# Optimization experiments

Hardware: AMD Instinct MI355X
Metric: run time of the kernel (lower is better)

## Reference

```python
import jax, jax.numpy as jnp
import numpy as np

N, S, D, H, E, ETYPES = 1024, 64, 256, 4, 4096, 4
HD = D // H
EPS = 1e-5


def setup_inputs() -> dict:
    key = jax.random.key(0)
    ks = jax.random.split(key, 8)
    node_features = jax.random.normal(ks[0], (N, S, D), dtype=jnp.float32)
    lengths = jax.random.randint(ks[1], (N,), 1, S + 1)
    node_masks = (jnp.arange(S)[None, :] < lengths[:, None]).astype(jnp.float32)
    # unique edges (torch builds an adjacency matrix, so duplicates collapse)
    rng = np.random.default_rng(0)
    cand = rng.integers(0, N, size=(4 * E, 2))
    uniq = np.unique(cand, axis=0)
    assert uniq.shape[0] >= E
    perm = rng.permutation(uniq.shape[0])[:E]
    edge_index = jnp.asarray(uniq[perm].T, dtype=jnp.int64)  # [2, E]
    edge_type = jnp.asarray(rng.integers(1, ETYPES + 1, size=(E,)), dtype=jnp.int64)
    scale = 0.02
    wq = jax.random.normal(ks[2], (D, D), jnp.float32) * scale
    wk = jax.random.normal(ks[3], (D, D), jnp.float32) * scale
    wv = jax.random.normal(ks[4], (D, D), jnp.float32) * scale
    wo = jax.random.normal(ks[5], (D, D), jnp.float32) * scale
    return dict(
        node_features=node_features, node_masks=node_masks,
        ln_w=jnp.ones((D,), jnp.float32), ln_b=jnp.zeros((D,), jnp.float32),
        wq=wq, bq=jnp.zeros((D,), jnp.float32),
        wk=wk, bk=jnp.zeros((D,), jnp.float32),
        wv=wv, bv=jnp.zeros((D,), jnp.float32),
        wo=wo, bo=jnp.zeros((D,), jnp.float32),
        edge_type_weights=jnp.ones((ETYPES,), jnp.float32),
        edge_index=edge_index, edge_type=edge_type,
    )


def reference(node_features, node_masks, ln_w, ln_b, wq, bq, wk, bk, wv, bv,
              wo, bo, edge_type_weights, edge_index, edge_type):
    n, s, d = node_features.shape
    # LayerNorm (biased variance, eps=1e-5, as torch)
    mu = jnp.mean(node_features, axis=-1, keepdims=True)
    var = jnp.mean((node_features - mu) ** 2, axis=-1, keepdims=True)
    xn = (node_features - mu) * jax.lax.rsqrt(var + EPS) * ln_w + ln_b
    q = (xn @ wq + bq).reshape(n, s, H, HD)
    k = (xn @ wk + bk).reshape(n, s, H, HD)
    v = (xn @ wv + bv).reshape(n, s, H, HD)
    src, dst = edge_index[0], edge_index[1]
    # per-edge scalar bias: softplus(edge_type_weights[type-1]).clamp(1e-6, 1e6)
    ew = jnp.clip(jax.nn.softplus(edge_type_weights[edge_type - 1]), 1e-6, 1e6)  # [E]
    qe, ke, ve = q[src], k[dst], v[dst]              # [E,S,H,HD]
    km = node_masks[dst]                              # [E,S] key-side mask
    qm = node_masks[src]                              # [E,S] query-side mask
    scores = jnp.einsum('eqhd,ekhd->ehqk', qe, ke) / jnp.sqrt(jnp.float32(HD))
    scores = scores + ew[:, None, None, None]
    neg = jnp.float32(-1e30)
    scores = jnp.where(km[:, None, None, :] > 0, scores, neg)
    # per-edge softmax over the key node's valid tokens; zero rows where no valid key
    attn = jax.nn.softmax(scores, axis=-1) * km[:, None, None, :]
    ctx = jnp.einsum('ehqk,ekhd->eqhd', attn, ve) * qm[:, :, None, None]  # [E,S,H,HD]
    out = jax.ops.segment_sum(ctx, src, num_segments=n)   # sum over incident edges
    out = out.reshape(n, s, d)
    out = out @ wo + bo                                   # output projection (dropout=eval noop)
    out = out + node_features                             # residual
    return out * node_masks[..., None]
```

## Files before the change

### kernel.cpp

```cpp
#include <hip/hip_runtime.h>

#define DDIM 256
#define NEDGE 4096
#define SLEN 64
#define NNODE 1024
#define ROWS 65536

typedef short s16x8 __attribute__((ext_vector_type(8)));
typedef float f32x4 __attribute__((ext_vector_type(4)));

static __device__ __forceinline__ unsigned short f2bf(float f){
  union { float f; unsigned u; } v; v.f = f;
  unsigned r = v.u + 0x7FFFu + ((v.u >> 16) & 1u);
  return (unsigned short)(r >> 16);
}

static __device__ __forceinline__ void gl2lds16(const unsigned short* g, unsigned short* l){
  __builtin_amdgcn_global_load_lds((const __attribute__((address_space(1))) unsigned int*)g,
                                   (__attribute__((address_space(3))) unsigned int*)l, 16, 0, 0);
}

__global__ __launch_bounds__(256) void setup_kernel(const float* nf, const float* lnw, const float* lnb,
                                                    const float* wq, const float* wk, const float* wv, const float* wo,
                                                    const float* bq, const float* bk, const float* bv,
                                                    const float* masks, const int* eidx,
                                                    unsigned short* xn, unsigned short* Wqkv, unsigned short* Wo_t,
                                                    float* qkvb, int* lenp, int* startp, int* order, int* degp, int* elist){
  __shared__ int deg[NNODE];
  __shared__ int buf[256];
  __shared__ int hist[65];
  __shared__ int cur[NNODE];
  int bid = blockIdx.x, tid = threadIdx.x;
  if (bid < 16384){
    int lane = tid & 63;
    int row = bid*4 + (tid >> 6);
    const float4 x4 = ((const float4*)(nf + (size_t)row*DDIM))[lane];
    float s  = x4.x + x4.y + x4.z + x4.w;
    float sq = x4.x*x4.x + x4.y*x4.y + x4.z*x4.z + x4.w*x4.w;
    for (int off=1; off<64; off<<=1){ s += __shfl_xor(s, off); sq += __shfl_xor(sq, off); }
    float mu  = s  * (1.0f/DDIM);
    float var = sq * (1.0f/DDIM) - mu*mu;
    float rs  = rsqrtf(var + 1e-5f);
    float4 w4 = ((const float4*)lnw)[lane];
    float4 b4 = ((const float4*)lnb)[lane];
    ushort4 o;
    o.x = f2bf((x4.x - mu)*rs*w4.x + b4.x);
    o.y = f2bf((x4.y - mu)*rs*w4.y + b4.y);
    o.z = f2bf((x4.z - mu)*rs*w4.z + b4.z);
    o.w = f2bf((x4.w - mu)*rs*w4.w + b4.w);
    ((ushort4*)(xn + (size_t)row*DDIM))[lane] = o;
  } else if (bid < 17412){
    int idx = (bid - 16384)*256 + tid;
    if (idx < 196608){
      int mat = idx >> 16;
      int rem = idx & 65535;
      int n = rem >> 8, k = rem & 255;
      const float* W = (mat==0)?wq:(mat==1)?wk:wv;
      Wqkv[(size_t)(mat*256 + n)*256 + k] = f2bf(W[k*256 + n]);
    } else if (idx < 262144){
      int rem = idx - 196608;
      int n = rem >> 8, k = rem & 255;
      Wo_t[(size_t)n*256 + k] = f2bf(wo[k*256 + n]);
    } else if (idx < 262912){
      int i = idx - 262144;
      qkvb[i] = (i < 256) ? bq[i] : (i < 512) ? bk[i-256] : bv[i-512];
    }
  } else if (bid < 17668){
    int lane = tid & 63;
    int node = (bid - 17412)*4 + (tid >> 6);
    unsigned long long b = __ballot(masks[node*SLEN + lane] > 0.f);
    if (lane == 0) lenp[node] = __popcll(b);
  } else {
    int t = tid;
    #pragma unroll
    for (int i=0;i<4;i++) deg[i*256 + t] = 0;
    if (t < 65) hist[t] = 0;
    __syncthreads();
    #pragma unroll
    for (int i=0;i<16;i++) atomicAdd(&deg[eidx[i*256 + t]], 1);
    __syncthreads();
    int d[4]; int s = 0;
    #pragma unroll
    for (int j=0;j<4;j++){ d[j] = deg[t*4 + j]; s += d[j]; }
    buf[t] = s;
    __syncthreads();
    for (int off=1; off<256; off<<=1){
      int v = (t >= off) ? buf[t-off] : 0;
      __syncthreads();
      buf[t] += v;
      __syncthreads();
    }
    int run = buf[t] - s;
    #pragma unroll
    for (int j=0;j<4;j++){
      int node = t*4 + j;
      startp[node] = run; degp[node] = d[j]; cur[node] = run;
      run += d[j];
      int dc = d[j] > 64 ? 64 : d[j];
      atomicAdd(&hist[dc], 1);
    }
    __syncthreads();
    if (t == 0){
      int acc = 0;
      for (int i=64;i>=0;i--){ int h = hist[i]; hist[i] = acc; acc += h; }
    }
    __syncthreads();
    #pragma unroll
    for (int j=0;j<4;j++){
      int node = t*4 + j;
      int dc = d[j] > 64 ? 64 : d[j];
      int pos = atomicAdd(&hist[dc], 1);
      order[pos] = node;
    }
    __syncthreads();
    #pragma unroll
    for (int i=0;i<16;i++){
      int e = i*256 + t;
      int sn = eidx[e];
      int p = atomicAdd(&cur[sn], 1);
      elist[p] = eidx[NEDGE + e];
    }
  }
}

__global__ __launch_bounds__(256) void qkv_kernel(const unsigned short* xn, const unsigned short* Wqkv,
                                                  const float* qkvb, const int* lenp,
                                                  unsigned short* qb, unsigned short* kb_, unsigned short* vt){
  __shared__ __align__(16) unsigned short As[2][8192];
  __shared__ __align__(16) unsigned short Bs[2][8192];
  int tid = threadIdx.x;
  int lane = tid & 63, wid = tid >> 6, m = lane & 15, quad = lane >> 4;
  int row0 = blockIdx.x * 128;
  int nodeA = row0 >> 6;
  int vraA = ((lenp[nodeA]   + 15) >> 4) << 4;
  int vraB = ((lenp[nodeA+1] + 15) >> 4) << 4;
  int col0 = blockIdx.y * 128;
  int wr = wid & 1, wc = wid >> 1;
  int rbase = wr * 64;
  int nodeW = nodeA + wr;
  int qtmW = (wr ? vraB : vraA) >> 4;

  f32x4 acc[16];
  #pragma unroll
  for (int i=0;i<16;i++) acc[i] = (f32x4){0.f,0.f,0.f,0.f};

  #pragma unroll
  for (int i=0;i<4;i++){
    int rowg = i*32 + wid*8;
    bool ok = (rowg < 64) ? (rowg < vraA) : (rowg - 64 < vraB);
    if (ok){
      int cid = i*256 + tid, row = cid >> 3, c8 = cid & 7;
      gl2lds16(xn + (size_t)(row0 + row)*DDIM + ((c8 ^ (row&7))<<3), As[0] + cid*8);
    }
  }
  #pragma unroll
  for (int i=0;i<4;i++){
    int cid = i*256 + tid, row = cid >> 3, c8 = cid & 7;
    gl2lds16(Wqkv + (size_t)(col0 + row)*DDIM + ((c8 ^ (row&7))<<3), Bs[0] + cid*8);
  }

  for (int kc = 0; kc < 4; kc++){
    __syncthreads();
    if (kc < 3){
      int kn = kc + 1;
      #pragma unroll
      for (int i=0;i<4;i++){
        int rowg = i*32 + wid*8;
        bool ok = (rowg < 64) ? (rowg < vraA) : (rowg - 64 < vraB);
        if (ok){
          int cid = i*256 + tid, row = cid >> 3, c8 = cid & 7;
          gl2lds16(xn + (size_t)(row0 + row)*DDIM + kn*64 + ((c8 ^ (row&7))<<3), As[kn&1] + cid*8);
        }
      }
      #pragma unroll
      for (int i=0;i<4;i++){
        int cid = i*256 + tid, row = cid >> 3, c8 = cid & 7;
        gl2lds16(Wqkv + (size_t)(col0 + row)*DDIM + kn*64 + ((c8 ^ (row&7))<<3), Bs[kn&1] + cid*8);
      }
    }
    const unsigned short* Asc = As[kc&1];
    const unsigned short* Bsc = Bs[kc&1];
    #pragma unroll
    for (int ks=0; ks<2; ks++){
      int sw = ((ks*4 + quad) ^ (m&7)) << 3;
      s16x8 af[4], bf[4];
      #pragma unroll
      for (int mt=0;mt<4;mt++) if (mt < qtmW) af[mt] = *(const s16x8*)(Asc + (rbase + mt*16 + m)*64 + sw);
      #pragma unroll
      for (int nt=0;nt<4;nt++) bf[nt] = *(const s16x8*)(Bsc + (wc*64 + nt*16 + m)*64 + sw);
      #pragma unroll
      for (int mt=0;mt<4;mt++) if (mt < qtmW)
        #pragma unroll
        for (int nt=0;nt<4;nt++)
          acc[mt*4+nt] = __builtin_amdgcn_mfma_f32_16x16x32_bf16(af[mt], bf[nt], acc[mt*4+nt], 0,0,0);
    }
  }
  #pragma unroll
  for (int nt=0;nt<4;nt++){
    int cg = col0 + wc*64 + nt*16 + m;
    int mat = cg >> 8, col = cg & 255;
    float bb = qkvb[cg];
    if (mat < 2){
      unsigned short* ob = (mat==0)?qb:kb_;
      #pragma unroll
      for (int mt=0;mt<4;mt++) if (mt < qtmW)
        #pragma unroll
        for (int r=0;r<4;r++){
          int row = row0 + rbase + mt*16 + quad*4 + r;
          ob[(size_t)row*DDIM + col] = f2bf(acc[mt*4+nt][r] + bb);
        }
    } else {
      #pragma unroll
      for (int mt=0;mt<4;mt++) if (mt < qtmW){
        int tok0 = mt*16 + quad*4;
        ushort4 p;
        p.x = f2bf(acc[mt*4+nt][0] + bb);
        p.y = f2bf(acc[mt*4+nt][1] + bb);
        p.z = f2bf(acc[mt*4+nt][2] + bb);
        p.w = f2bf(acc[mt*4+nt][3] + bb);
        *(ushort4*)(vt + ((size_t)nodeW*256 + col)*64 + tok0) = p;
      }
    }
  }
}

__global__ __launch_bounds__(256) void attn_kernel(const unsigned short* qb, const unsigned short* kbuf,
                                                   const unsigned short* vtb, const int* lenp,
                                                   const int* startp, const int* degp, const int* elist,
                                                   const int* order, unsigned short* ctxb){
  __shared__ unsigned short P[4096];
  int tid = threadIdx.x;
  int lane = tid & 63, wid = tid >> 6, m = lane & 15, quad = lane >> 4;
  int src = order[blockIdx.x], h = blockIdx.y;
  int qtm = (lenp[src] + 15) >> 4;
  if (wid >= qtm) return;
  int s0 = startp[src], dg = degp[src];
  unsigned short* Pw = P + wid*1024;

  const unsigned short* qbase = qb + (size_t)(src*SLEN + wid*16 + m)*DDIM + h*64 + quad*8;
  s16x8 qf0 = *(const s16x8*)(qbase);
  s16x8 qf1 = *(const s16x8*)(qbase + 32);
  f32x4 o[4];
  #pragma unroll
  for (int i=0;i<4;i++) o[i] = (f32x4){0.f,0.f,0.f,0.f};

  int dstc = 0, ldc = 0;
  if (dg > 0){ dstc = elist[s0]; ldc = lenp[dstc]; }
  for (int ei=0; ei<dg; ei++){
    int dstn = 0, ldn = 0;
    if (ei+1 < dg){ dstn = elist[s0+ei+1]; ldn = lenp[dstn]; }
    int ktm = (ldc + 15) >> 4;
    int ks2 = (ktm + 1) >> 1;
    const unsigned short* kb0 = kbuf + (size_t)dstc*SLEN*DDIM + h*64 + quad*8;
    const unsigned short* vb0 = vtb + ((size_t)dstc*256 + h*64)*64;

    f32x4 acc[4];
    #pragma unroll
    for (int i=0;i<4;i++) acc[i] = (f32x4){0.f,0.f,0.f,0.f};
    #pragma unroll
    for (int kt=0; kt<4; kt++) if (kt < ktm){
      int key = kt*16 + m;
      s16x8 b0 = *(const s16x8*)(kb0 + (size_t)key*DDIM);
      s16x8 b1 = *(const s16x8*)(kb0 + (size_t)key*DDIM + 32);
      acc[kt] = __builtin_amdgcn_mfma_f32_16x16x32_bf16(qf0, b0, acc[kt], 0,0,0);
      acc[kt] = __builtin_amdgcn_mfma_f32_16x16x32_bf16(qf1, b1, acc[kt], 0,0,0);
    }
    #pragma unroll
    for (int r=0; r<4; r++){
      float x[4];
      #pragma unroll
      for (int kt=0; kt<4; kt++)
        x[kt] = (kt < ktm && kt*16 + m < ldc) ? __expf(acc[kt][r]*0.125f) : 0.f;
      float s = x[0] + x[1] + x[2] + x[3];
      for (int off=1; off<16; off<<=1) s += __shfl_xor(s, off);
      float inv = 1.0f / s;
      int q = quad*4 + r;
      #pragma unroll
      for (int kt=0; kt<4; kt++) if (kt < 2*ks2){
        int key = kt*16 + m;
        Pw[q*64 + (((key>>3)^(q&7))<<3) + (key&7)] = f2bf(x[kt]*inv);
      }
    }
    #pragma unroll
    for (int ks=0; ks<2; ks++) if (ks < ks2){
      s16x8 pa = *(const s16x8*)(Pw + m*64 + (((ks*4+quad)^(m&7))<<3));
      #pragma unroll
      for (int dt=0; dt<4; dt++){
        s16x8 vf = *(const s16x8*)(vb0 + (dt*16 + m)*64 + (ks*4+quad)*8);
        o[dt] = __builtin_amdgcn_mfma_f32_16x16x32_bf16(pa, vf, o[dt], 0,0,0);
      }
    }
    dstc = dstn; ldc = ldn;
  }
  #pragma unroll
  for (int dt=0; dt<4; dt++){
    int col = h*64 + dt*16 + m;
    #pragma unroll
    for (int r=0; r<4; r++){
      int row = src*SLEN + wid*16 + quad*4 + r;
      ctxb[(size_t)row*DDIM + col] = f2bf(o[dt][r]);
    }
  }
}

__global__ __launch_bounds__(256) void out_kernel(const unsigned short* ctxb, const unsigned short* Wo_t,
                                                  const float* bo, const float* nf, const float* masks,
                                                  const int* lenp, float* out){
  __shared__ __align__(16) unsigned short As[2][8192];
  __shared__ __align__(16) unsigned short Bs[2][8192];
  int tid = threadIdx.x;
  int lane = tid & 63, wid = tid >> 6, m = lane & 15, quad = lane >> 4;
  int row0 = blockIdx.x * 128;
  int nodeA = row0 >> 6;
  int vraA = ((lenp[nodeA]   + 15) >> 4) << 4;
  int vraB = ((lenp[nodeA+1] + 15) >> 4) << 4;
  int col0 = blockIdx.y * 128;
  int wr = wid & 1, wc = wid >> 1;
  int rbase = wr * 64;
  int qtmW = (wr ? vraB : vraA) >> 4;

  f32x4 acc[16];
  #pragma unroll
  for (int i=0;i<16;i++) acc[i] = (f32x4){0.f,0.f,0.f,0.f};

  #pragma unroll
  for (int i=0;i<4;i++){
    int rowg = i*32 + wid*8;
    bool ok = (rowg < 64) ? (rowg < vraA) : (rowg - 64 < vraB);
    if (ok){
      int cid = i*256 + tid, row = cid >> 3, c8 = cid & 7;
      gl2lds16(ctxb + (size_t)(row0 + row)*DDIM + ((c8 ^ (row&7))<<3), As[0] + cid*8);
    }
  }
  #pragma unroll
  for (int i=0;i<4;i++){
    int cid = i*256 + tid, row = cid >> 3, c8 = cid & 7;
    gl2lds16(Wo_t + (size_t)(col0 + row)*DDIM + ((c8 ^ (row&7))<<3), Bs[0] + cid*8);
  }

  for (int kc = 0; kc < 4; kc++){
    __syncthreads();
    if (kc < 3){
      int kn = kc + 1;
      #pragma unroll
      for (int i=0;i<4;i++){
        int rowg = i*32 + wid*8;
        bool ok = (rowg < 64) ? (rowg < vraA) : (rowg - 64 < vraB);
        if (ok){
          int cid = i*256 + tid, row = cid >> 3, c8 = cid & 7;
          gl2lds16(ctxb + (size_t)(row0 + row)*DDIM + kn*64 + ((c8 ^ (row&7))<<3), As[kn&1] + cid*8);
        }
      }
      #pragma unroll
      for (int i=0;i<4;i++){
        int cid = i*256 + tid, row = cid >> 3, c8 = cid & 7;
        gl2lds16(Wo_t + (size_t)(col0 + row)*DDIM + kn*64 + ((c8 ^ (row&7))<<3), Bs[kn&1] + cid*8);
      }
    }
    const unsigned short* Asc = As[kc&1];
    const unsigned short* Bsc = Bs[kc&1];
    #pragma unroll
    for (int ks=0; ks<2; ks++){
      int sw = ((ks*4 + quad) ^ (m&7)) << 3;
      s16x8 af[4], bf[4];
      #pragma unroll
      for (int mt=0;mt<4;mt++) if (mt < qtmW) af[mt] = *(const s16x8*)(Asc + (rbase + mt*16 + m)*64 + sw);
      #pragma unroll
      for (int nt=0;nt<4;nt++) bf[nt] = *(const s16x8*)(Bsc + (wc*64 + nt*16 + m)*64 + sw);
      #pragma unroll
      for (int mt=0;mt<4;mt++) if (mt < qtmW)
        #pragma unroll
        for (int nt=0;nt<4;nt++)
          acc[mt*4+nt] = __builtin_amdgcn_mfma_f32_16x16x32_bf16(af[mt], bf[nt], acc[mt*4+nt], 0,0,0);
    }
  }
  #pragma unroll
  for (int nt=0;nt<4;nt++){
    int col = col0 + wc*64 + nt*16 + m;
    float bb = bo[col];
    #pragma unroll
    for (int mt=0;mt<4;mt++){
      if (mt < qtmW){
        #pragma unroll
        for (int r=0;r<4;r++){
          int row = row0 + rbase + mt*16 + quad*4 + r;
          float v = acc[mt*4+nt][r] + bb + nf[(size_t)row*DDIM + col];
          out[(size_t)row*DDIM + col] = v * masks[row];
        }
      } else {
        #pragma unroll
        for (int r=0;r<4;r++){
          int row = row0 + rbase + mt*16 + quad*4 + r;
          out[(size_t)row*DDIM + col] = 0.f;
        }
      }
    }
  }
}

extern "C" void kernel_launch(void* const* d_in, const int* in_sizes, int n_in,
                              void* d_out, int out_size, void* d_ws, size_t ws_size,
                              hipStream_t stream){
  const float* nf    = (const float*)d_in[0];
  const float* masks = (const float*)d_in[1];
  const float* lnw   = (const float*)d_in[2];
  const float* lnb   = (const float*)d_in[3];
  const float* wq    = (const float*)d_in[4];
  const float* bq    = (const float*)d_in[5];
  const float* wk    = (const float*)d_in[6];
  const float* bk    = (const float*)d_in[7];
  const float* wv    = (const float*)d_in[8];
  const float* bv    = (const float*)d_in[9];
  const float* wo    = (const float*)d_in[10];
  const float* bo    = (const float*)d_in[11];
  const int*   eidx  = (const int*)d_in[13];
  float* out = (float*)d_out;

  char* ws = (char*)d_ws;
  const size_t B = (size_t)ROWS * DDIM * 2;
  unsigned short* xn   = (unsigned short*)(ws);
  unsigned short* qb   = (unsigned short*)(ws + B);
  unsigned short* kb   = (unsigned short*)(ws + 2*B);
  unsigned short* vt   = (unsigned short*)(ws + 3*B);
  unsigned short* ctxb = (unsigned short*)(ws + 4*B);
  char* wp = ws + 5*B;
  unsigned short* Wqkv = (unsigned short*)(wp);
  unsigned short* Wo_t = (unsigned short*)(wp + 393216);
  float* qkvb         = (float*)(wp + 524288);
  char* ip = wp + 528384;
  int* startp = (int*)(ip);
  int* lenp   = (int*)(ip + 4096);
  int* order  = (int*)(ip + 8192);
  int* degp   = (int*)(ip + 12288);
  int* elist  = (int*)(ip + 16384);

  setup_kernel<<<17669, 256, 0, stream>>>(nf, lnw, lnb, wq, wk, wv, wo, bq, bk, bv,
                                          masks, eidx, xn, Wqkv, Wo_t, qkvb,
                                          lenp, startp, order, degp, elist);
  qkv_kernel<<<dim3(ROWS/128, 6), 256, 0, stream>>>(xn, Wqkv, qkvb, lenp, qb, kb, vt);
  attn_kernel<<<dim3(NNODE, 4), 256, 0, stream>>>(qb, kb, vt, lenp, startp, degp, elist, order, ctxb);
  out_kernel<<<dim3(ROWS/128, 2), 256, 0, stream>>>(ctxb, Wo_t, bo, nf, masks, lenp, out);
}
```

Measured before the change: 353.2 us.

## Stage per-edge K/V tiles in LDS with async multi-buffered prefetch

The attention kernel used to read K and V fragments for each neighbour edge straight from global memory in every wave. Now the whole block cooperatively copies each edge's K tile (triple-buffered) and V^T tile (double-buffered) into swizzled LDS with global_load_lds, prefetching upcoming edges while the current one is computed. Inactive waves stay alive to help with loading and barriers, and s_setprio is raised around the MFMA section. The intent is to share loads across the four query waves and hide global latency. The cost is about 40 KB of extra LDS per block, which lowers occupancy, plus a block-wide barrier per edge.

After: 361.5 us. 1.02x slower.

```diff
diff --git a/kernel.cpp b/kernel.cpp
--- a/kernel.cpp
+++ b/kernel.cpp
@@ -228,77 +228,127 @@
                                                    const unsigned short* vtb, const int* lenp,
                                                    const int* startp, const int* degp, const int* elist,
                                                    const int* order, unsigned short* ctxb){
+  __shared__ __align__(16) unsigned short Kt[3][4096];
+  __shared__ __align__(16) unsigned short Vt[2][4096];
   __shared__ unsigned short P[4096];
   int tid = threadIdx.x;
   int lane = tid & 63, wid = tid >> 6, m = lane & 15, quad = lane >> 4;
   int src = order[blockIdx.x], h = blockIdx.y;
   int qtm = (lenp[src] + 15) >> 4;
-  if (wid >= qtm) return;
   int s0 = startp[src], dg = degp[src];
+  bool active = wid < qtm;
   unsigned short* Pw = P + wid*1024;
 
-  const unsigned short* qbase = qb + (size_t)(src*SLEN + wid*16 + m)*DDIM + h*64 + quad*8;
-  s16x8 qf0 = *(const s16x8*)(qbase);
-  s16x8 qf1 = *(const s16x8*)(qbase + 32);
+  s16x8 qf0 = {0,0,0,0,0,0,0,0}, qf1 = {0,0,0,0,0,0,0,0};
+  if (active){
+    const unsigned short* qbase = qb + (size_t)(src*SLEN + wid*16 + m)*DDIM + h*64 + quad*8;
+    qf0 = *(const s16x8*)(qbase);
+    qf1 = *(const s16x8*)(qbase + 32);
+  }
   f32x4 o[4];
   #pragma unroll
   for (int i=0;i<4;i++) o[i] = (f32x4){0.f,0.f,0.f,0.f};
 
-  int dstc = 0, ldc = 0;
-  if (dg > 0){ dstc = elist[s0]; ldc = lenp[dstc]; }
-  for (int ei=0; ei<dg; ei++){
-    int dstn = 0, ldn = 0;
-    if (ei+1 < dg){ dstn = elist[s0+ei+1]; ldn = lenp[dstn]; }
-    int ktm = (ldc + 15) >> 4;
+#define STAGE_K(dstn, bufi) do{ \
+    const unsigned short* kp_ = kbuf + (size_t)(dstn)*SLEN*DDIM + h*64; \
+    _Pragma("unroll") \
+    for (int i_=0;i_<2;i_++){ \
+      int cid_ = i_*256 + tid, row_ = cid_ >> 3, c8_ = cid_ & 7; \
+      gl2lds16(kp_ + (size_t)row_*DDIM + ((c8_ ^ (row_&7))<<3), Kt[bufi] + cid_*8); \
+    } }while(0)
+#define STAGE_V(dstn, bufi) do{ \
+    const unsigned short* vp_ = vtb + ((size_t)(dstn)*256 + h*64)*64; \
+    _Pragma("unroll") \
+    for (int i_=0;i_<2;i_++){ \
+      int cid_ = i_*256 + tid, row_ = cid_ >> 3, c8_ = cid_ & 7; \
+      gl2lds16(vp_ + row_*64 + ((c8_ ^ (row_&7))<<3), Vt[bufi] + cid_*8); \
+    } }while(0)
+
+  int dst0 = 0, dst1 = 0, ld0 = 0, ld1 = 0;
+  if (dg > 0){
+    dst0 = elist[s0]; ld0 = lenp[dst0];
+    STAGE_K(dst0, 0);
+    STAGE_V(dst0, 0);
+  }
+  if (dg > 1){
+    dst1 = elist[s0 + 1]; ld1 = lenp[dst1];
+    STAGE_K(dst1, 1);
+    asm volatile("s_waitcnt vmcnt(2)" ::: "memory");
+  } else {
+    asm volatile("s_waitcnt vmcnt(0)" ::: "memory");
+  }
+  __builtin_amdgcn_s_barrier();
+
+  int cur = 0;
+  for (int ei = 0; ei < dg; ei++){
+    if (ei + 1 < dg) STAGE_V(dst1, (ei+1)&1);
+    int dst2 = 0, ld2 = 0;
+    bool pf = (ei + 2 < dg);
+    if (pf){
+      dst2 = elist[s0 + ei + 2]; ld2 = lenp[dst2];
+      int kbn = (cur == 0) ? 2 : cur - 1;
+      STAGE_K(dst2, kbn);
+    }
+    int ktm = (ld0 + 15) >> 4;
     int ks2 = (ktm + 1) >> 1;
-    const unsigned short* kb0 = kbuf + (size_t)dstc*SLEN*DDIM + h*64 + quad*8;
-    const unsigned short* vb0 = vtb + ((size_t)dstc*256 + h*64)*64;
-
-    f32x4 acc[4];
-    #pragma unroll
-    for (int i=0;i<4;i++) acc[i] = (f32x4){0.f,0.f,0.f,0.f};
-    #pragma unroll
-    for (int kt=0; kt<4; kt++) if (kt < ktm){
-      int key = kt*16 + m;
-      s16x8 b0 = *(const s16x8*)(kb0 + (size_t)key*DDIM);
-      s16x8 b1 = *(const s16x8*)(kb0 + (size_t)key*DDIM + 32);
-      acc[kt] = __builtin_amdgcn_mfma_f32_16x16x32_bf16(qf0, b0, acc[kt], 0,0,0);
-      acc[kt] = __builtin_amdgcn_mfma_f32_16x16x32_bf16(qf1, b1, acc[kt], 0,0,0);
-    }
-    #pragma unroll
-    for (int r=0; r<4; r++){
-      float x[4];
-      #pragma unroll
-      for (int kt=0; kt<4; kt++)
-        x[kt] = (kt < ktm && kt*16 + m < ldc) ? __expf(acc[kt][r]*0.125f) : 0.f;
-      float s = x[0] + x[1] + x[2] + x[3];
-      for (int off=1; off<16; off<<=1) s += __shfl_xor(s, off);
-      float inv = 1.0f / s;
-      int q = quad*4 + r;
-      #pragma unroll
-      for (int kt=0; kt<4; kt++) if (kt < 2*ks2){
+    if (active){
+      __builtin_amdgcn_s_setprio(1);
+      f32x4 acc[4];
+      #pragma unroll
+      for (int i=0;i<4;i++) acc[i] = (f32x4){0.f,0.f,0.f,0.f};
+      #pragma unroll
+      for (int kt=0; kt<4; kt++) if (kt < ktm){
         int key = kt*16 + m;
-        Pw[q*64 + (((key>>3)^(q&7))<<3) + (key&7)] = f2bf(x[kt]*inv);
-      }
-    }
-    #pragma unroll
-    for (int ks=0; ks<2; ks++) if (ks < ks2){
-      s16x8 pa = *(const s16x8*)(Pw + m*64 + (((ks*4+quad)^(m&7))<<3));
-      #pragma unroll
-      for (int dt=0; dt<4; dt++){
-        s16x8 vf = *(const s16x8*)(vb0 + (dt*16 + m)*64 + (ks*4+quad)*8);
-        o[dt] = __builtin_amdgcn_mfma_f32_16x16x32_bf16(pa, vf, o[dt], 0,0,0);
-      }
-    }
-    dstc = dstn; ldc = ldn;
-  }
-  #pragma unroll
-  for (int dt=0; dt<4; dt++){
-    int col = h*64 + dt*16 + m;
-    #pragma unroll
-    for (int r=0; r<4; r++){
-      int row = src*SLEN + wid*16 + quad*4 + r;
-      ctxb[(size_t)row*DDIM + col] = f2bf(o[dt][r]);
+        s16x8 b0 = *(const s16x8*)(Kt[cur] + key*64 + ((quad ^ (m&7))<<3));
+        acc[kt] = __builtin_amdgcn_mfma_f32_16x16x32_bf16(qf0, b0, acc[kt], 0,0,0);
+        s16x8 b1 = *(const s16x8*)(Kt[cur] + key*64 + (((4 + quad) ^ (m&7))<<3));
+        acc[kt] = __builtin_amdgcn_mfma_f32_16x16x32_bf16(qf1, b1, acc[kt], 0,0,0);
+      }
+      #pragma unroll
+      for (int r=0; r<4; r++){
+        float x[4];
+        #pragma unroll
+        for (int kt=0; kt<4; kt++)
+          x[kt] = (kt < ktm && kt*16 + m < ld0) ? __expf(acc[kt][r]*0.125f) : 0.f;
+        float s = x[0] + x[1] + x[2] + x[3];
+        for (int off=1; off<16; off<<=1) s += __shfl_xor(s, off);
+        float inv = 1.0f / s;
+        int q = quad*4 + r;
+        #pragma unroll
+        for (int kt=0; kt<4; kt++) if (kt < 2*ks2){
+          int key = kt*16 + m;
+          Pw[q*64 + (((key>>3)^(q&7))<<3) + (key&7)] = f2bf(x[kt]*inv);
+        }
+      }
+      #pragma unroll
+      for (int ks=0; ks<2; ks++) if (ks < ks2){
+        s16x8 pa = *(const s16x8*)(Pw + m*64 + (((ks*4+quad)^(m&7))<<3));
+        #pragma unroll
+        for (int dt=0; dt<4; dt++){
+          int d = dt*16 + m;
+          s16x8 vf = *(const s16x8*)(Vt[ei&1] + d*64 + (((ks*4+quad)^(d&7))<<3));
+          o[dt] = __builtin_amdgcn_mfma_f32_16x16x32_bf16(pa, vf, o[dt], 0,0,0);
+        }
+      }
+      __builtin_amdgcn_s_setprio(0);
+    }
+    if (pf) asm volatile("s_waitcnt vmcnt(2)" ::: "memory");
+    else    asm volatile("s_waitcnt vmcnt(0)" ::: "memory");
+    __builtin_amdgcn_s_barrier();
+    dst0 = dst1; ld0 = ld1; dst1 = dst2; ld1 = ld2;
+    cur = (cur == 2) ? 0 : cur + 1;
+  }
+#undef STAGE_K
+#undef STAGE_V
+  if (active){
+    #pragma unroll
+    for (int dt=0; dt<4; dt++){
+      int col = h*64 + dt*16 + m;
+      #pragma unroll
+      for (int r=0; r<4; r++){
+        int row = src*SLEN + wid*16 + quad*4 + r;
+        ctxb[(size_t)row*DDIM + col] = f2bf(o[dt][r]);
+      }
     }
   }
 }
```

## Map heads to waves and reuse K/V fragments across all query tiles

Applied to the files above, without the earlier changes.

The attention kernel changes from one block per (source node, head), with one wave per query tile, to one block per source node, with one wave per head. Each wave loops over all query tiles of its head, so each edge's K and V fragments are loaded from global memory once per wave and reused across up to four query tiles. The next edge's K fragments are prefetched into registers while the current edge is being computed. In exchange, each wave holds far more registers (launch_bounds(256,2)), the grid has a quarter as many blocks, and the per-wave work is serialised.

Measured after the change: 349.5 us. About the same (-1.1%).

```diff
diff --git a/kernel.cpp b/kernel.cpp
--- a/kernel.cpp
+++ b/kernel.cpp
@@ -224,81 +224,121 @@
   }
 }
 
-__global__ __launch_bounds__(256) void attn_kernel(const unsigned short* qb, const unsigned short* kbuf,
-                                                   const unsigned short* vtb, const int* lenp,
-                                                   const int* startp, const int* degp, const int* elist,
-                                                   const int* order, unsigned short* ctxb){
+__global__ __launch_bounds__(256, 2) void attn_kernel(const unsigned short* qb, const unsigned short* kbuf,
+                                                      const unsigned short* vtb, const int* lenp,
+                                                      const int* startp, const int* degp, const int* elist,
+                                                      const int* order, unsigned short* ctxb){
   __shared__ unsigned short P[4096];
   int tid = threadIdx.x;
   int lane = tid & 63, wid = tid >> 6, m = lane & 15, quad = lane >> 4;
-  int src = order[blockIdx.x], h = blockIdx.y;
+  int src = order[blockIdx.x], h = wid;
   int qtm = (lenp[src] + 15) >> 4;
-  if (wid >= qtm) return;
   int s0 = startp[src], dg = degp[src];
   unsigned short* Pw = P + wid*1024;
 
-  const unsigned short* qbase = qb + (size_t)(src*SLEN + wid*16 + m)*DDIM + h*64 + quad*8;
-  s16x8 qf0 = *(const s16x8*)(qbase);
-  s16x8 qf1 = *(const s16x8*)(qbase + 32);
-  f32x4 o[4];
-  #pragma unroll
-  for (int i=0;i<4;i++) o[i] = (f32x4){0.f,0.f,0.f,0.f};
-
-  int dstc = 0, ldc = 0;
-  if (dg > 0){ dstc = elist[s0]; ldc = lenp[dstc]; }
+  s16x8 qf0[4], qf1[4];
+  #pragma unroll
+  for (int qt=0; qt<4; qt++){
+    if (qt < qtm){
+      const unsigned short* qbase = qb + (size_t)(src*SLEN + qt*16 + m)*DDIM + h*64 + quad*8;
+      qf0[qt] = *(const s16x8*)(qbase);
+      qf1[qt] = *(const s16x8*)(qbase + 32);
+    } else {
+      qf0[qt] = (s16x8){0,0,0,0,0,0,0,0};
+      qf1[qt] = (s16x8){0,0,0,0,0,0,0,0};
+    }
+  }
+  f32x4 o[4][4];
+  #pragma unroll
+  for (int qt=0; qt<4; qt++)
+    #pragma unroll
+    for (int dt=0; dt<4; dt++) o[qt][dt] = (f32x4){0.f,0.f,0.f,0.f};
+
+  s16x8 kf[8];
+  #pragma unroll
+  for (int i=0;i<8;i++) kf[i] = (s16x8){0,0,0,0,0,0,0,0};
+  int dst0 = 0, ld0 = 0;
+  if (dg > 0){
+    dst0 = elist[s0]; ld0 = lenp[dst0];
+    const unsigned short* kb0 = kbuf + (size_t)dst0*SLEN*DDIM + h*64 + quad*8;
+    #pragma unroll
+    for (int kt=0; kt<4; kt++){
+      int key = kt*16 + m;
+      kf[kt*2]   = *(const s16x8*)(kb0 + (size_t)key*DDIM);
+      kf[kt*2+1] = *(const s16x8*)(kb0 + (size_t)key*DDIM + 32);
+    }
+  }
+
   for (int ei=0; ei<dg; ei++){
-    int dstn = 0, ldn = 0;
-    if (ei+1 < dg){ dstn = elist[s0+ei+1]; ldn = lenp[dstn]; }
-    int ktm = (ldc + 15) >> 4;
+    s16x8 vf[8];
+    const unsigned short* vb0 = vtb + ((size_t)dst0*256 + h*64)*64;
+    #pragma unroll
+    for (int ks=0; ks<2; ks++)
+      #pragma unroll
+      for (int dt=0; dt<4; dt++)
+        vf[ks*4+dt] = *(const s16x8*)(vb0 + (dt*16 + m)*64 + (ks*4+quad)*8);
+    s16x8 kn[8];
+    int dst1 = 0, ld1 = 0;
+    if (ei+1 < dg){
+      dst1 = elist[s0 + ei + 1]; ld1 = lenp[dst1];
+      const unsigned short* kb1 = kbuf + (size_t)dst1*SLEN*DDIM + h*64 + quad*8;
+      #pragma unroll
+      for (int kt=0; kt<4; kt++){
+        int key = kt*16 + m;
+        kn[kt*2]   = *(const s16x8*)(kb1 + (size_t)key*DDIM);
+        kn[kt*2+1] = *(const s16x8*)(kb1 + (size_t)key*DDIM + 32);
+      }
+    }
+    int ktm = (ld0 + 15) >> 4;
     int ks2 = (ktm + 1) >> 1;
-    const unsigned short* kb0 = kbuf + (size_t)dstc*SLEN*DDIM + h*64 + quad*8;
-    const unsigned short* vb0 = vtb + ((size_t)dstc*256 + h*64)*64;
-
-    f32x4 acc[4];
-    #pragma unroll
-    for (int i=0;i<4;i++) acc[i] = (f32x4){0.f,0.f,0.f,0.f};
-    #pragma unroll
-    for (int kt=0; kt<4; kt++) if (kt < ktm){
-      int key = kt*16 + m;
-      s16x8 b0 = *(const s16x8*)(kb0 + (size_t)key*DDIM);
-      s16x8 b1 = *(const s16x8*)(kb0 + (size_t)key*DDIM + 32);
-      acc[kt] = __builtin_amdgcn_mfma_f32_16x16x32_bf16(qf0, b0, acc[kt], 0,0,0);
-      acc[kt] = __builtin_amdgcn_mfma_f32_16x16x32_bf16(qf1, b1, acc[kt], 0,0,0);
-    }
-    #pragma unroll
-    for (int r=0; r<4; r++){
-      float x[4];
-      #pragma unroll
-      for (int kt=0; kt<4; kt++)
-        x[kt] = (kt < ktm && kt*16 + m < ldc) ? __expf(acc[kt][r]*0.125f) : 0.f;
-      float s = x[0] + x[1] + x[2] + x[3];
-      for (int off=1; off<16; off<<=1) s += __shfl_xor(s, off);
-      float inv = 1.0f / s;
-      int q = quad*4 + r;
-      #pragma unroll
-      for (int kt=0; kt<4; kt++) if (kt < 2*ks2){
-        int key = kt*16 + m;
-        Pw[q*64 + (((key>>3)^(q&7))<<3) + (key&7)] = f2bf(x[kt]*inv);
-      }
-    }
-    #pragma unroll
-    for (int ks=0; ks<2; ks++) if (ks < ks2){
-      s16x8 pa = *(const s16x8*)(Pw + m*64 + (((ks*4+quad)^(m&7))<<3));
-      #pragma unroll
-      for (int dt=0; dt<4; dt++){
-        s16x8 vf = *(const s16x8*)(vb0 + (dt*16 + m)*64 + (ks*4+quad)*8);
-        o[dt] = __builtin_amdgcn_mfma_f32_16x16x32_bf16(pa, vf, o[dt], 0,0,0);
-      }
-    }
-    dstc = dstn; ldc = ldn;
-  }
-  #pragma unroll
-  for (int dt=0; dt<4; dt++){
-    int col = h*64 + dt*16 + m;
-    #pragma unroll
-    for (int r=0; r<4; r++){
-      int row = src*SLEN + wid*16 + quad*4 + r;
-      ctxb[(size_t)row*DDIM + col] = f2bf(o[dt][r]);
+    #pragma unroll
+    for (int qt=0; qt<4; qt++) if (qt < qtm){
+      f32x4 acc[4];
+      #pragma unroll
+      for (int i=0;i<4;i++) acc[i] = (f32x4){0.f,0.f,0.f,0.f};
+      #pragma unroll
+      for (int kt=0; kt<4; kt++) if (kt < ktm){
+        acc[kt] = __builtin_amdgcn_mfma_f32_16x16x32_bf16(qf0[qt], kf[kt*2],   acc[kt], 0,0,0);
+        acc[kt] = __builtin_amdgcn_mfma_f32_16x16x32_bf16(qf1[qt], kf[kt*2+1], acc[kt], 0,0,0);
+      }
+      #pragma unroll
+      for (int r=0; r<4; r++){
+        float x[4];
+        #pragma unroll
+        for (int kt=0; kt<4; kt++)
+          x[kt] = (kt < ktm && kt*16 + m < ld0) ? __expf(acc[kt][r]*0.125f) : 0.f;
+        float s = x[0] + x[1] + x[2] + x[3];
+        for (int off=1; off<16; off<<=1) s += __shfl_xor(s, off);
+        float inv = 1.0f / s;
+        int q = quad*4 + r;
+        #pragma unroll
+        for (int kt=0; kt<4; kt++) if (kt < 2*ks2){
+          int key = kt*16 + m;
+          Pw[q*64 + (((key>>3)^(q&7))<<3) + (key&7)] = f2bf(x[kt]*inv);
+        }
+      }
+      #pragma unroll
+      for (int ks=0; ks<2; ks++) if (ks < ks2){
+        s16x8 pa = *(const s16x8*)(Pw + m*64 + (((ks*4+quad)^(m&7))<<3));
+        #pragma unroll
+        for (int dt=0; dt<4; dt++)
+          o[qt][dt] = __builtin_amdgcn_mfma_f32_16x16x32_bf16(pa, vf[ks*4+dt], o[qt][dt], 0,0,0);
+      }
+    }
+    dst0 = dst1; ld0 = ld1;
+    #pragma unroll
+    for (int i=0;i<8;i++) kf[i] = kn[i];
+  }
+  #pragma unroll
+  for (int qt=0; qt<4; qt++) if (qt < qtm){
+    #pragma unroll
+    for (int dt=0; dt<4; dt++){
+      int col = h*64 + dt*16 + m;
+      #pragma unroll
+      for (int r=0; r<4; r++){
+        int row = src*SLEN + qt*16 + quad*4 + r;
+        ctxb[(size_t)row*DDIM + col] = f2bf(o[qt][dt][r]);
+      }
     }
   }
 }
@@ -438,6 +478,6 @@
                                           masks, eidx, xn, Wqkv, Wo_t, qkvb,
                                           lenp, startp, order, degp, elist);
   qkv_kernel<<<dim3(ROWS/128, 6), 256, 0, stream>>>(xn, Wqkv, qkvb, lenp, qb, kb, vt);
-  attn_kernel<<<dim3(NNODE, 4), 256, 0, stream>>>(qb, kb, vt, lenp, startp, degp, elist, order, ctxb);
+  attn_kernel<<<NNODE, 256, 0, stream>>>(qb, kb, vt, lenp, startp, degp, elist, order, ctxb);
   out_kernel<<<dim3(ROWS/128, 2), 256, 0, stream>>>(ctxb, Wo_t, bo, nf, masks, lenp, out);
 }
```
